# Optimization experiments

Hardware: AMD Instinct MI355X
Metric: run time of the kernel (lower is better)

The kernel has to match this reference:

```python
import jax, jax.numpy as jnp
import numpy as np

Q_BITS = 8
GELU_A = -0.2888
GELU_B = -1.769
INV_SQRT2 = 0.7071067811865476


def _ste_round(x):
    # straight-through round (identity grad)
    return x + jax.lax.stop_gradient(jnp.round(x) - x)


def fake_quant_weight(w):
    # per-tensor symmetric int8 fake quant
    qmax = 2.0 ** (Q_BITS - 1) - 1.0  # 127
    s = jnp.maximum(jnp.max(jnp.abs(w)), 1e-8) / qmax
    q = jnp.clip(_ste_round(w / s), -qmax - 1.0, qmax)
    return q * s


def fake_quant_act(x):
    # per-tensor asymmetric uint8 fake quant
    levels = 2.0 ** Q_BITS - 1.0  # 255
    xmin = jax.lax.stop_gradient(jnp.min(x))
    xmax = jax.lax.stop_gradient(jnp.max(x))
    s = jnp.maximum(xmax - xmin, 1e-8) / levels
    zp = jnp.round(-xmin / s)
    q = jnp.clip(_ste_round(x / s) + zp, 0.0, levels)
    return (q - zp) * s


def int_gelu(x):
    # I-BERT polynomial GELU: gelu(x) = x * 0.5 * (1 + L(x/sqrt(2)))
    # L(t) = sign(t) * (a * (clip(|t|, 0, -b) + b)^2 + 1)
    t = x * INV_SQRT2
    at = jnp.minimum(jnp.abs(t), -GELU_B)
    L = jnp.sign(t) * (GELU_A * (at + GELU_B) ** 2 + 1.0)
    return x * 0.5 * (1.0 + L)


def setup_inputs() -> dict:
    key = jax.random.key(0)
    k = jax.random.split(key, 5)
    B, S, D, H = 64, 197, 768, 3072
    x = jax.random.normal(k[0], (B, S, D), dtype=jnp.float32)
    w1 = jax.random.normal(k[1], (H, D), dtype=jnp.float32) * (1.0 / np.sqrt(D))
    b1 = jax.random.normal(k[2], (H,), dtype=jnp.float32) * 0.02
    w2 = jax.random.normal(k[3], (D, H), dtype=jnp.float32) * (1.0 / np.sqrt(H))
    b2 = jax.random.normal(k[4], (D,), dtype=jnp.float32) * 0.02
    return {"x": x, "w1": w1, "b1": b1, "w2": w2, "b2": b2}


def reference(x, w1, b1, w2, b2):
    # QuantLinear 1: fake-quant act + weight, then GEMM
    xq = fake_quant_act(x)
    h = jnp.einsum('bsd,hd->bsh', xq, fake_quant_weight(w1)) + b1
    # IntGELU (dropout is identity in eval)
    g = int_gelu(h)
    # QuantLinear 2
    gq = fake_quant_act(g)
    out = jnp.einsum('bsh,dh->bsd', gq, fake_quant_weight(w2)) + b2
    return out
```

## Files before the change

kernel.cpp:

```cpp
#include <hip/hip_runtime.h>
#include <stdint.h>
#include <stddef.h>

typedef int v4i  __attribute__((ext_vector_type(4)));
typedef int v16i __attribute__((ext_vector_type(16)));
typedef _Float16 vh8 __attribute__((ext_vector_type(8)));

#define GELU_A   (-0.2888f)
#define GELU_B   (-1.769f)
#define INV_SQRT2 0.70710678118654752440f

#define GLD16(gp, lp) __builtin_amdgcn_global_load_lds( \
    (const __attribute__((address_space(1))) unsigned int*)(gp), \
    (__attribute__((address_space(3))) unsigned int*)(lp), 16, 0, 0)

#define WAIT_VM4 0x0F74
#define WAIT_VM0 0x0F70


__device__ __forceinline__ unsigned enc_f(float f){
  unsigned u = __float_as_uint(f);
  return (u & 0x80000000u) ? ~u : (u | 0x80000000u);
}
__device__ __forceinline__ float dec_f(unsigned e){
  unsigned u = (e & 0x80000000u) ? (e & 0x7FFFFFFFu) : ~e;
  return __uint_as_float(u);
}

__device__ __forceinline__ float int_gelu_f(float x){
  float t = x * INV_SQRT2;
  float at = fminf(fabsf(t), 1.769f);
  float u = at + GELU_B;
  float p = GELU_A * (u * u) + 1.0f;
  float L = (t > 0.0f) ? p : ((t < 0.0f) ? -p : 0.0f);
  return x * 0.5f * (1.0f + L);
}

__global__ __launch_bounds__(256) void reduce_stats(
    const float4* __restrict__ x, int nx4,
    const float4* __restrict__ w1, int n14,
    const float4* __restrict__ w2, int n24,
    unsigned* __restrict__ sc)
{
  __shared__ float ra[256], rb[256];
  const int tid = threadIdx.x;
  const int b = blockIdx.x;
  if (b < 1024){
    float lmin = 3.4e38f, lmax = -3.4e38f;
    for (long i = (long)b * 256 + tid; i < nx4; i += 1024L * 256L){
      float4 v = x[i];
      lmin = fminf(lmin, fminf(fminf(v.x, v.y), fminf(v.z, v.w)));
      lmax = fmaxf(lmax, fmaxf(fmaxf(v.x, v.y), fmaxf(v.z, v.w)));
    }
    ra[tid] = lmin; rb[tid] = lmax;
    __syncthreads();
    for (int s = 128; s > 0; s >>= 1){
      if (tid < s){ ra[tid] = fminf(ra[tid], ra[tid + s]); rb[tid] = fmaxf(rb[tid], rb[tid + s]); }
      __syncthreads();
    }
    if (tid == 0){
      atomicMin(&sc[0], enc_f(ra[0]));
      atomicMax(&sc[2], enc_f(rb[0]));
    }
  } else {
    const float4* w; int n4; int slot; int bl;
    if (b < 1152){ w = w1; n4 = n14; slot = 3; bl = b - 1024; }
    else         { w = w2; n4 = n24; slot = 4; bl = b - 1152; }
    float la = 0.0f;
    for (long i = (long)bl * 256 + tid; i < n4; i += 128L * 256L){
      float4 v = w[i];
      la = fmaxf(la, fmaxf(fmaxf(fabsf(v.x), fabsf(v.y)), fmaxf(fabsf(v.z), fabsf(v.w))));
    }
    ra[tid] = la;
    __syncthreads();
    for (int s = 128; s > 0; s >>= 1){
      if (tid < s) ra[tid] = fmaxf(ra[tid], ra[tid + s]);
      __syncthreads();
    }
    if (tid == 0) atomicMax(&sc[slot], __float_as_uint(ra[0]));
  }
}

__global__ __launch_bounds__(256) void quant_all(
    const float4* __restrict__ x, unsigned* __restrict__ qx, long nx4,
    const float* __restrict__ w1, const float* __restrict__ w2,
    int8_t* __restrict__ qw1, int8_t* __restrict__ qw2,
    int* __restrict__ rs1, int* __restrict__ rs2,
    const unsigned* __restrict__ sc, int H, int D)
{
  const int tid = threadIdx.x;
  const int b = blockIdx.x;
  if (b < 2048){
    const float vmin = dec_f(sc[0]);
    const float vmax = dec_f(sc[2]);
    const float s  = fmaxf(vmax - vmin, 1e-8f) / 255.0f;
    const float zp = rintf(-vmin / s);
    for (long i = (long)b * 256 + tid; i < nx4; i += 2048L * 256L){
      float4 v = x[i];
      int q0 = (int)fminf(fmaxf(rintf(v.x / s) + zp, 0.0f), 255.0f) - 128;
      int q1 = (int)fminf(fmaxf(rintf(v.y / s) + zp, 0.0f), 255.0f) - 128;
      int q2 = (int)fminf(fmaxf(rintf(v.z / s) + zp, 0.0f), 255.0f) - 128;
      int q3 = (int)fminf(fmaxf(rintf(v.w / s) + zp, 0.0f), 255.0f) - 128;
      qx[i] = ((unsigned)(q0 & 255)) | ((unsigned)(q1 & 255) << 8) |
              ((unsigned)(q2 & 255) << 16) | ((unsigned)(q3 & 255) << 24);
    }
  } else {
    __shared__ int red[256];
    const int wb = b - 2048;
    const float* w; int8_t* q; int* rs; int K; int n; float s;
    if (wb < H){ w = w1; q = qw1; rs = rs1; K = D; n = wb;
                 s = fmaxf(__uint_as_float(sc[3]), 1e-8f) / 127.0f; }
    else       { w = w2; q = qw2; rs = rs2; K = H; n = wb - H;
                 s = fmaxf(__uint_as_float(sc[4]), 1e-8f) / 127.0f; }
    int sum = 0;
    for (int k = tid; k < K; k += 256){
      float v = w[(size_t)n * K + k];
      float qf = fminf(fmaxf(rintf(v / s), -128.0f), 127.0f);
      int qi = (int)qf;
      q[(size_t)n * K + k] = (int8_t)qi;
      sum += qi;
    }
    red[tid] = sum;
    __syncthreads();
    for (int st = 128; st > 0; st >>= 1){
      if (tid < st) red[tid] += red[tid + st];
      __syncthreads();
    }
    if (tid == 0) rs[n] = red[0];
  }
}

__global__ __launch_bounds__(256) void quant_g(
    const vh8* __restrict__ g, uint2* __restrict__ qg, long n8,
    const unsigned* __restrict__ sc)
{
  const float gmin = dec_f(sc[1]), gmax = dec_f(sc[5]);
  const float qs  = fmaxf(gmax - gmin, 1e-8f) / 255.0f;
  const float qzp = rintf(-gmin / qs);
  const long stride = (long)gridDim.x * blockDim.x;
  for (long i = (long)blockIdx.x * blockDim.x + threadIdx.x; i < n8; i += stride){
    vh8 v = g[i];
    unsigned lo = 0, hi = 0;
#pragma unroll
    for (int j = 0; j < 4; j++){
      int q = (int)fminf(fmaxf(rintf((float)v[j] / qs) + qzp, 0.0f), 255.0f) - 128;
      lo |= ((unsigned)(q & 255)) << (8 * j);
    }
#pragma unroll
    for (int j = 0; j < 4; j++){
      int q = (int)fminf(fmaxf(rintf((float)v[4 + j] / qs) + qzp, 0.0f), 255.0f) - 128;
      hi |= ((unsigned)(q & 255)) << (8 * j);
    }
    uint2 o; o.x = lo; o.y = hi;
    qg[i] = o;
  }
}

template<int MODE>
__global__ __launch_bounds__(256) void gemm_i8(
    const int8_t* __restrict__ A, const int8_t* __restrict__ Bm,
    const int* __restrict__ rowsum, const float* __restrict__ bias,
    void* __restrict__ Cout, int M, int N, int K,
    unsigned* __restrict__ sc)
{
  __shared__ __align__(16) int8_t lds[3][16384];

  const int tid  = threadIdx.x;
  const int lane = tid & 63;
  const int wave = tid >> 6;
  const int l31  = lane & 31;
  const int kh   = lane >> 5;
  const int n0   = blockIdx.x * 128;
  const int m0   = blockIdx.y * 128;
  const int wm   = (wave & 1) * 64;
  const int wn   = (wave >> 1) * 64;

  int aoffs[2], boffs[2];
  const int ldst[2] = { wave * 2048, wave * 2048 + 1024 };
#pragma unroll
  for (int t = 0; t < 2; t++){
    int rowl = wave * 32 + t * 16 + (lane >> 2);
    int csw  = ((lane & 3) ^ ((rowl >> 1) & 3)) << 4;
    int ga = m0 + rowl; if (ga >= M) ga = M - 1;
    aoffs[t] = ga * K + csw;
    boffs[t] = (n0 + rowl) * K + csw;
  }

  const int w2  = (l31 >> 1) & 3;
  const int sA0 = (kh ^ w2) << 4;
  int arow[2], brow[2];
#pragma unroll
  for (int mi = 0; mi < 2; mi++){
    arow[mi] = (wm + mi * 32 + l31) * 64;
    brow[mi] = (wn + mi * 32 + l31) * 64;
  }

  v16i acc[2][2] = {};
  const int NT = K >> 6;

#pragma unroll
  for (int t = 0; t < 2; t++){
    GLD16(A  + aoffs[t],      &lds[0][ldst[t]]);
    GLD16(Bm + boffs[t],      &lds[0][8192 + ldst[t]]);
  }
#pragma unroll
  for (int t = 0; t < 2; t++){
    GLD16(A  + aoffs[t] + 64, &lds[1][ldst[t]]);
    GLD16(Bm + boffs[t] + 64, &lds[1][8192 + ldst[t]]);
  }

  for (int kt = 0; kt < NT; kt++){
    const int8_t* buf = lds[kt % 3];
    if (kt + 1 < NT) __builtin_amdgcn_s_waitcnt(WAIT_VM4);
    else             __builtin_amdgcn_s_waitcnt(WAIT_VM0);
    __builtin_amdgcn_s_barrier();
    __builtin_amdgcn_sched_barrier(0);

    v4i af[2][2], bf[2][2];
#pragma unroll
    for (int kk = 0; kk < 2; kk++){
      const int sb = sA0 ^ (kk << 5);
#pragma unroll
      for (int mi = 0; mi < 2; mi++){
        af[kk][mi] = *(const v4i*)(buf + arow[mi] + sb);
        bf[kk][mi] = *(const v4i*)(buf + 8192 + brow[mi] + sb);
      }
    }

    if (kt + 2 < NT){
      int8_t* nbuf = lds[(kt + 2) % 3];
      const int ko = (kt + 2) << 6;
#pragma unroll
      for (int t = 0; t < 2; t++){
        GLD16(A  + aoffs[t] + ko, nbuf + ldst[t]);
        GLD16(Bm + boffs[t] + ko, nbuf + 8192 + ldst[t]);
      }
    }

#pragma unroll
    for (int kk = 0; kk < 2; kk++)
#pragma unroll
      for (int mi = 0; mi < 2; mi++)
#pragma unroll
        for (int nj = 0; nj < 2; nj++)
          acc[mi][nj] = __builtin_amdgcn_mfma_i32_32x32x32_i8(af[kk][mi], bf[kk][nj], acc[mi][nj], 0, 0, 0);
  }

  float s_h, off_h;
  if constexpr (MODE == 1){
    float gmin = dec_f(sc[1]), gmax = dec_f(sc[5]);
    float sg = fmaxf(gmax - gmin, 1e-8f) / 255.0f;
    float zp = rintf(-gmin / sg);
    float sw = fmaxf(__uint_as_float(sc[4]), 1e-8f) / 127.0f;
    s_h = sg * sw; off_h = 128.0f - zp;
  } else {
    float xmin = dec_f(sc[0]), xmax = dec_f(sc[2]);
    float sx = fmaxf(xmax - xmin, 1e-8f) / 255.0f;
    float zp = rintf(-xmin / sx);
    float sw = fmaxf(__uint_as_float(sc[3]), 1e-8f) / 127.0f;
    s_h = sx * sw; off_h = 128.0f - zp;
  }
  float qs = 1.0f, qzp = 0.0f;
  if constexpr (MODE == 2){
    float gmin = dec_f(sc[1]), gmax = dec_f(sc[5]);
    qs = fmaxf(gmax - gmin, 1e-8f) / 255.0f;
    qzp = rintf(-gmin / qs);
  }

  float lmin = 3.4e38f, lmax = -3.4e38f;
#pragma unroll
  for (int nj = 0; nj < 2; nj++){
    const int n = n0 + wn + nj * 32 + l31;
    const float rsv = off_h * (float)rowsum[n];
    const float bv = bias[n];
#pragma unroll
    for (int mi = 0; mi < 2; mi++){
      const int mbase = m0 + wm + mi * 32 + 4 * kh;
#pragma unroll
      for (int r = 0; r < 16; r++){
        const int m = mbase + (r & 3) + 8 * (r >> 2);
        if (m < M){
          float h = s_h * ((float)acc[mi][nj][r] + rsv) + bv;
          if constexpr (MODE == 0){
            float gv = int_gelu_f(h);
            lmin = fminf(lmin, gv); lmax = fmaxf(lmax, gv);
          } else if constexpr (MODE == 3){
            float gv = int_gelu_f(h);
            lmin = fminf(lmin, gv); lmax = fmaxf(lmax, gv);
            ((_Float16*)Cout)[(size_t)m * N + n] = (_Float16)gv;
          } else if constexpr (MODE == 2){
            float gv = int_gelu_f(h);
            float qf = fminf(fmaxf(rintf(gv / qs) + qzp, 0.0f), 255.0f);
            ((int8_t*)Cout)[(size_t)m * N + n] = (int8_t)((int)qf - 128);
          } else {
            ((float*)Cout)[(size_t)m * N + n] = h;
          }
        }
      }
    }
  }

  if constexpr (MODE == 0 || MODE == 3){
    __syncthreads();
    float* redA = (float*)&lds[0][0];
    float* redB = ((float*)&lds[0][0]) + 256;
    redA[tid] = lmin; redB[tid] = lmax;
    __syncthreads();
    for (int st = 128; st > 0; st >>= 1){
      if (tid < st){
        redA[tid] = fminf(redA[tid], redA[tid + st]);
        redB[tid] = fmaxf(redB[tid], redB[tid + st]);
      }
      __syncthreads();
    }
    if (tid == 0){
      atomicMin(&sc[1], enc_f(redA[0]));
      atomicMax(&sc[5], enc_f(redB[0]));
    }
  }
}

extern "C" void kernel_launch(void* const* d_in, const int* in_sizes, int n_in,
                              void* d_out, int out_size, void* d_ws, size_t ws_size,
                              hipStream_t stream)
{
  const float* x  = (const float*)d_in[0];
  const float* w1 = (const float*)d_in[1];
  const float* b1 = (const float*)d_in[2];
  const float* w2 = (const float*)d_in[3];
  const float* b2 = (const float*)d_in[4];
  float* out = (float*)d_out;

  const int H = in_sizes[2];
  const int D = in_sizes[4];
  const int M = in_sizes[0] / D;

  char* ws = (char*)d_ws;
  unsigned* sc = (unsigned*)ws;
  size_t off = 256;
  int8_t* qx  = (int8_t*)(ws + off); off += (size_t)M * D;
  int8_t* qw1 = (int8_t*)(ws + off); off += (size_t)H * D;
  int8_t* qw2 = (int8_t*)(ws + off); off += (size_t)D * H;
  int* rs1 = (int*)(ws + off); off += (size_t)H * 4;
  int* rs2 = (int*)(ws + off); off += 4096;
  int8_t* qg  = (int8_t*)(ws + off); off += (size_t)M * H;
  _Float16* g16 = (_Float16*)(ws + off);
  const size_t need_big = off + (size_t)M * H * 2;
  (void)n_in; (void)out_size;

  hipMemsetAsync(sc, 0xFF, 8, stream);
  hipMemsetAsync(sc + 2, 0x00, 16, stream);

  reduce_stats<<<dim3(1280), dim3(256), 0, stream>>>(
      (const float4*)x, M * D / 4,
      (const float4*)w1, H * D / 4,
      (const float4*)w2, D * H / 4, sc);

  quant_all<<<dim3(2048 + H + D), dim3(256), 0, stream>>>(
      (const float4*)x, (unsigned*)qx, (long)M * D / 4,
      w1, w2, qw1, qw2, rs1, rs2, sc, H, D);

  const dim3 g1(H / 128, (M + 127) / 128), g2(D / 128, (M + 127) / 128), blk(256);

  if (ws_size >= need_big){
    gemm_i8<3><<<g1, blk, 0, stream>>>(qx, qw1, rs1, b1, g16, M, H, D, sc);
    quant_g<<<dim3(2048), blk, 0, stream>>>(
        (const vh8*)g16, (uint2*)qg, (long)M * H / 8, sc);
  } else {
    gemm_i8<0><<<g1, blk, 0, stream>>>(qx, qw1, rs1, b1, nullptr, M, H, D, sc);
    gemm_i8<2><<<g1, blk, 0, stream>>>(qx, qw1, rs1, b1, qg, M, H, D, sc);
  }

  gemm_i8<1><<<g2, blk, 0, stream>>>(qg, qw2, rs2, b2, out, M, D, H, sc);
}
```

Before: 309.3 us.

## Widen int8 GEMM block tile to 128x256 with 64x128 per-wave subtiles

Doubles the N extent of each GEMM block tile from 128 to 256, so each wave computes a 64x128 output subtile with a 2x4 array of MFMA accumulators. B-tile loads per stage double and the LDS triple buffer grows to 24 KB per stage, with the vmcnt wait adjusted for the six outstanding loads. The aim is more reuse of each A fragment and a higher MFMA-to-LDS-read ratio. In exchange the grid is half as large, accumulator register use doubles, and occupancy may drop, which could leave CUs idle on the 768-wide second GEMM.

```diff
diff --git a/kernel.cpp b/kernel.cpp
--- a/kernel.cpp
+++ b/kernel.cpp
@@ -14,7 +14,7 @@
     (const __attribute__((address_space(1))) unsigned int*)(gp), \
     (__attribute__((address_space(3))) unsigned int*)(lp), 16, 0, 0)
 
-#define WAIT_VM4 0x0F74
+#define WAIT_VM6 0x0F76
 #define WAIT_VM0 0x0F70
 
 
@@ -157,84 +157,88 @@
 }
 
 template<int MODE>
-__global__ __launch_bounds__(256) void gemm_i8(
+__global__ __launch_bounds__(256, 2) void gemm_i8(
     const int8_t* __restrict__ A, const int8_t* __restrict__ Bm,
     const int* __restrict__ rowsum, const float* __restrict__ bias,
     void* __restrict__ Cout, int M, int N, int K,
     unsigned* __restrict__ sc)
 {
-  __shared__ __align__(16) int8_t lds[3][16384];
+  __shared__ __align__(16) int8_t lds[3][24576];
 
   const int tid  = threadIdx.x;
   const int lane = tid & 63;
   const int wave = tid >> 6;
   const int l31  = lane & 31;
   const int kh   = lane >> 5;
-  const int n0   = blockIdx.x * 128;
+  const int n0   = blockIdx.x * 256;
   const int m0   = blockIdx.y * 128;
-  const int wm   = (wave & 1) * 64;
-  const int wn   = (wave >> 1) * 64;
-
-  int aoffs[2], boffs[2];
-  const int ldst[2] = { wave * 2048, wave * 2048 + 1024 };
+  const int wm   = (wave >> 1) * 64;
+  const int wn   = (wave & 1) * 128;
+
+  int aoffs[2], boffs[4];
+  const int ldstA[2] = { wave * 2048, wave * 2048 + 1024 };
+  const int ldstB[4] = { 8192 + wave * 4096,        8192 + wave * 4096 + 1024,
+                         8192 + wave * 4096 + 2048, 8192 + wave * 4096 + 3072 };
 #pragma unroll
   for (int t = 0; t < 2; t++){
     int rowl = wave * 32 + t * 16 + (lane >> 2);
     int csw  = ((lane & 3) ^ ((rowl >> 1) & 3)) << 4;
     int ga = m0 + rowl; if (ga >= M) ga = M - 1;
     aoffs[t] = ga * K + csw;
+  }
+#pragma unroll
+  for (int t = 0; t < 4; t++){
+    int rowl = wave * 64 + t * 16 + (lane >> 2);
+    int csw  = ((lane & 3) ^ ((rowl >> 1) & 3)) << 4;
     boffs[t] = (n0 + rowl) * K + csw;
   }
 
   const int w2  = (l31 >> 1) & 3;
   const int sA0 = (kh ^ w2) << 4;
-  int arow[2], brow[2];
-#pragma unroll
-  for (int mi = 0; mi < 2; mi++){
-    arow[mi] = (wm + mi * 32 + l31) * 64;
-    brow[mi] = (wn + mi * 32 + l31) * 64;
-  }
-
-  v16i acc[2][2] = {};
+  int arow[2], brow[4];
+#pragma unroll
+  for (int mi = 0; mi < 2; mi++) arow[mi] = (wm + mi * 32 + l31) * 64;
+#pragma unroll
+  for (int nj = 0; nj < 4; nj++) brow[nj] = (wn + nj * 32 + l31) * 64;
+
+  v16i acc[2][4] = {};
   const int NT = K >> 6;
 
 #pragma unroll
-  for (int t = 0; t < 2; t++){
-    GLD16(A  + aoffs[t],      &lds[0][ldst[t]]);
-    GLD16(Bm + boffs[t],      &lds[0][8192 + ldst[t]]);
-  }
-#pragma unroll
-  for (int t = 0; t < 2; t++){
-    GLD16(A  + aoffs[t] + 64, &lds[1][ldst[t]]);
-    GLD16(Bm + boffs[t] + 64, &lds[1][8192 + ldst[t]]);
-  }
+  for (int t = 0; t < 2; t++) GLD16(A  + aoffs[t],      &lds[0][ldstA[t]]);
+#pragma unroll
+  for (int t = 0; t < 4; t++) GLD16(Bm + boffs[t],      &lds[0][ldstB[t]]);
+#pragma unroll
+  for (int t = 0; t < 2; t++) GLD16(A  + aoffs[t] + 64, &lds[1][ldstA[t]]);
+#pragma unroll
+  for (int t = 0; t < 4; t++) GLD16(Bm + boffs[t] + 64, &lds[1][ldstB[t]]);
 
   for (int kt = 0; kt < NT; kt++){
     const int8_t* buf = lds[kt % 3];
-    if (kt + 1 < NT) __builtin_amdgcn_s_waitcnt(WAIT_VM4);
+    if (kt + 1 < NT) __builtin_amdgcn_s_waitcnt(WAIT_VM6);
     else             __builtin_amdgcn_s_waitcnt(WAIT_VM0);
     __builtin_amdgcn_s_barrier();
     __builtin_amdgcn_sched_barrier(0);
 
-    v4i af[2][2], bf[2][2];
+    v4i af[2][2], bf[2][4];
 #pragma unroll
     for (int kk = 0; kk < 2; kk++){
       const int sb = sA0 ^ (kk << 5);
 #pragma unroll
-      for (int mi = 0; mi < 2; mi++){
+      for (int mi = 0; mi < 2; mi++)
         af[kk][mi] = *(const v4i*)(buf + arow[mi] + sb);
-        bf[kk][mi] = *(const v4i*)(buf + 8192 + brow[mi] + sb);
-      }
+#pragma unroll
+      for (int nj = 0; nj < 4; nj++)
+        bf[kk][nj] = *(const v4i*)(buf + 8192 + brow[nj] + sb);
     }
 
     if (kt + 2 < NT){
       int8_t* nbuf = lds[(kt + 2) % 3];
       const int ko = (kt + 2) << 6;
 #pragma unroll
-      for (int t = 0; t < 2; t++){
-        GLD16(A  + aoffs[t] + ko, nbuf + ldst[t]);
-        GLD16(Bm + boffs[t] + ko, nbuf + 8192 + ldst[t]);
-      }
+      for (int t = 0; t < 2; t++) GLD16(A  + aoffs[t] + ko, nbuf + ldstA[t]);
+#pragma unroll
+      for (int t = 0; t < 4; t++) GLD16(Bm + boffs[t] + ko, nbuf + ldstB[t]);
     }
 
 #pragma unroll
@@ -242,7 +246,7 @@
 #pragma unroll
       for (int mi = 0; mi < 2; mi++)
 #pragma unroll
-        for (int nj = 0; nj < 2; nj++)
+        for (int nj = 0; nj < 4; nj++)
           acc[mi][nj] = __builtin_amdgcn_mfma_i32_32x32x32_i8(af[kk][mi], bf[kk][nj], acc[mi][nj], 0, 0, 0);
   }
 
@@ -269,7 +273,7 @@
 
   float lmin = 3.4e38f, lmax = -3.4e38f;
 #pragma unroll
-  for (int nj = 0; nj < 2; nj++){
+  for (int nj = 0; nj < 4; nj++){
     const int n = n0 + wn + nj * 32 + l31;
     const float rsv = off_h * (float)rowsum[n];
     const float bv = bias[n];
@@ -360,7 +364,7 @@
       (const float4*)x, (unsigned*)qx, (long)M * D / 4,
       w1, w2, qw1, qw2, rs1, rs2, sc, H, D);
 
-  const dim3 g1(H / 128, (M + 127) / 128), g2(D / 128, (M + 127) / 128), blk(256);
+  const dim3 g1(H / 256, (M + 127) / 128), g2(D / 256, (M + 127) / 128), blk(256);
 
   if (ws_size >= need_big){
     gemm_i8<3><<<g1, blk, 0, stream>>>(qx, qw1, rs1, b1, g16, M, H, D, sc);
```

New measurement: 331.8 us. 7.3% more time.

## Pre-swizzle int8 operands into MFMA fragment layout and drop LDS staging

Applied to the files above, without the earlier changes.

Quantization kernels now write activations, weights and the intermediate GELU output in a blocked 32x32 fragment-native layout. This lets the GEMM load each lane's MFMA operands directly from global memory with 16-byte loads, removing the LDS triple-buffer, global-to-LDS copies and barriers. The K loop is double-buffered in registers and occupancy is hinted with launch bounds. The trade-off is that each wave reads its operands directly from global memory with no LDS sharing, so reuse depends on caches, and there is less latency hiding than with the LDS pipeline.

```diff
diff --git a/kernel.cpp b/kernel.cpp
--- a/kernel.cpp
+++ b/kernel.cpp
@@ -10,12 +10,6 @@
 #define GELU_B   (-1.769f)
 #define INV_SQRT2 0.70710678118654752440f
 
-#define GLD16(gp, lp) __builtin_amdgcn_global_load_lds( \
-    (const __attribute__((address_space(1))) unsigned int*)(gp), \
-    (__attribute__((address_space(3))) unsigned int*)(lp), 16, 0, 0)
-
-#define WAIT_VM4 0x0F74
-#define WAIT_VM0 0x0F70
 
 
 __device__ __forceinline__ unsigned enc_f(float f){
@@ -81,8 +75,17 @@
   }
 }
 
+__device__ __forceinline__ unsigned quant4_act(float4 v, float s, float zp){
+  int q0 = (int)fminf(fmaxf(rintf(v.x / s) + zp, 0.0f), 255.0f) - 128;
+  int q1 = (int)fminf(fmaxf(rintf(v.y / s) + zp, 0.0f), 255.0f) - 128;
+  int q2 = (int)fminf(fmaxf(rintf(v.z / s) + zp, 0.0f), 255.0f) - 128;
+  int q3 = (int)fminf(fmaxf(rintf(v.w / s) + zp, 0.0f), 255.0f) - 128;
+  return ((unsigned)(q0 & 255)) | ((unsigned)(q1 & 255) << 8) |
+         ((unsigned)(q2 & 255) << 16) | ((unsigned)(q3 & 255) << 24);
+}
+
 __global__ __launch_bounds__(256) void quant_all(
-    const float4* __restrict__ x, unsigned* __restrict__ qx, long nx4,
+    const float* __restrict__ x, int8_t* __restrict__ qx, long nchunk,
     const float* __restrict__ w1, const float* __restrict__ w2,
     int8_t* __restrict__ qw1, int8_t* __restrict__ qw2,
     int* __restrict__ rs1, int* __restrict__ rs2,
@@ -95,14 +98,19 @@
     const float vmax = dec_f(sc[2]);
     const float s  = fmaxf(vmax - vmin, 1e-8f) / 255.0f;
     const float zp = rintf(-vmin / s);
-    for (long i = (long)b * 256 + tid; i < nx4; i += 2048L * 256L){
-      float4 v = x[i];
-      int q0 = (int)fminf(fmaxf(rintf(v.x / s) + zp, 0.0f), 255.0f) - 128;
-      int q1 = (int)fminf(fmaxf(rintf(v.y / s) + zp, 0.0f), 255.0f) - 128;
-      int q2 = (int)fminf(fmaxf(rintf(v.z / s) + zp, 0.0f), 255.0f) - 128;
-      int q3 = (int)fminf(fmaxf(rintf(v.w / s) + zp, 0.0f), 255.0f) - 128;
-      qx[i] = ((unsigned)(q0 & 255)) | ((unsigned)(q1 & 255) << 8) |
-              ((unsigned)(q2 & 255) << 16) | ((unsigned)(q3 & 255) << 24);
+    const long CPR = (long)(D >> 4);
+    const long KB  = (long)(D >> 5);
+    for (long i = (long)b * 256 + tid; i < nchunk; i += 2048L * 256L){
+      long m = i / CPR; int c = (int)(i - m * CPR);
+      const float4* xp = (const float4*)(x + m * (long)D + (long)c * 16);
+      uint4 o;
+      o.x = quant4_act(xp[0], s, zp);
+      o.y = quant4_act(xp[1], s, zp);
+      o.z = quant4_act(xp[2], s, zp);
+      o.w = quant4_act(xp[3], s, zp);
+      size_t off = ((((size_t)(m >> 5)) * KB + (c >> 1)) << 10)
+                 + ((size_t)(c & 1) << 9) + ((m & 31) << 4);
+      *(uint4*)(qx + off) = o;
     }
   } else {
     __shared__ int red[256];
@@ -113,12 +121,25 @@
     else       { w = w2; q = qw2; rs = rs2; K = H; n = wb - H;
                  s = fmaxf(__uint_as_float(sc[4]), 1e-8f) / 127.0f; }
     int sum = 0;
-    for (int k = tid; k < K; k += 256){
-      float v = w[(size_t)n * K + k];
-      float qf = fminf(fmaxf(rintf(v / s), -128.0f), 127.0f);
-      int qi = (int)qf;
-      q[(size_t)n * K + k] = (int8_t)qi;
-      sum += qi;
+    const int c = tid;
+    if (c < (K >> 4)){
+      const float4* wp = (const float4*)(w + (size_t)n * K + (size_t)c * 16);
+      uint4 o; unsigned wds[4];
+#pragma unroll
+      for (int q4 = 0; q4 < 4; q4++){
+        float4 v = wp[q4];
+        int qa = (int)fminf(fmaxf(rintf(v.x / s), -128.0f), 127.0f);
+        int qb = (int)fminf(fmaxf(rintf(v.y / s), -128.0f), 127.0f);
+        int qc = (int)fminf(fmaxf(rintf(v.z / s), -128.0f), 127.0f);
+        int qd = (int)fminf(fmaxf(rintf(v.w / s), -128.0f), 127.0f);
+        sum += qa + qb + qc + qd;
+        wds[q4] = ((unsigned)(qa & 255)) | ((unsigned)(qb & 255) << 8) |
+                  ((unsigned)(qc & 255) << 16) | ((unsigned)(qd & 255) << 24);
+      }
+      o.x = wds[0]; o.y = wds[1]; o.z = wds[2]; o.w = wds[3];
+      size_t off = ((((size_t)(n >> 5)) * (K >> 5) + (c >> 1)) << 10)
+                 + ((size_t)(c & 1) << 9) + ((n & 31) << 4);
+      *(uint4*)(q + off) = o;
     }
     red[tid] = sum;
     __syncthreads();
@@ -131,40 +152,38 @@
 }
 
 __global__ __launch_bounds__(256) void quant_g(
-    const vh8* __restrict__ g, uint2* __restrict__ qg, long n8,
+    const vh8* __restrict__ gf, uint4* __restrict__ qg, long nchunk,
     const unsigned* __restrict__ sc)
 {
   const float gmin = dec_f(sc[1]), gmax = dec_f(sc[5]);
   const float qs  = fmaxf(gmax - gmin, 1e-8f) / 255.0f;
   const float qzp = rintf(-gmin / qs);
   const long stride = (long)gridDim.x * blockDim.x;
-  for (long i = (long)blockIdx.x * blockDim.x + threadIdx.x; i < n8; i += stride){
-    vh8 v = g[i];
-    unsigned lo = 0, hi = 0;
-#pragma unroll
-    for (int j = 0; j < 4; j++){
-      int q = (int)fminf(fmaxf(rintf((float)v[j] / qs) + qzp, 0.0f), 255.0f) - 128;
-      lo |= ((unsigned)(q & 255)) << (8 * j);
-    }
-#pragma unroll
-    for (int j = 0; j < 4; j++){
-      int q = (int)fminf(fmaxf(rintf((float)v[4 + j] / qs) + qzp, 0.0f), 255.0f) - 128;
-      hi |= ((unsigned)(q & 255)) << (8 * j);
-    }
-    uint2 o; o.x = lo; o.y = hi;
+  for (long i = (long)blockIdx.x * blockDim.x + threadIdx.x; i < nchunk; i += stride){
+    vh8 v0 = gf[2 * i], v1 = gf[2 * i + 1];
+    unsigned wds[4] = {0u, 0u, 0u, 0u};
+#pragma unroll
+    for (int j = 0; j < 8; j++){
+      int q = (int)fminf(fmaxf(rintf((float)v0[j] / qs) + qzp, 0.0f), 255.0f) - 128;
+      wds[j >> 2] |= ((unsigned)(q & 255)) << (8 * (j & 3));
+    }
+#pragma unroll
+    for (int j = 0; j < 8; j++){
+      int q = (int)fminf(fmaxf(rintf((float)v1[j] / qs) + qzp, 0.0f), 255.0f) - 128;
+      wds[2 + (j >> 2)] |= ((unsigned)(q & 255)) << (8 * (j & 3));
+    }
+    uint4 o; o.x = wds[0]; o.y = wds[1]; o.z = wds[2]; o.w = wds[3];
     qg[i] = o;
   }
 }
 
 template<int MODE>
-__global__ __launch_bounds__(256) void gemm_i8(
-    const int8_t* __restrict__ A, const int8_t* __restrict__ Bm,
+__global__ __launch_bounds__(256, 4) void gemm_i8f(
+    const int8_t* __restrict__ Af, const int8_t* __restrict__ Bf,
     const int* __restrict__ rowsum, const float* __restrict__ bias,
     void* __restrict__ Cout, int M, int N, int K,
     unsigned* __restrict__ sc)
 {
-  __shared__ __align__(16) int8_t lds[3][16384];
-
   const int tid  = threadIdx.x;
   const int lane = tid & 63;
   const int wave = tid >> 6;
@@ -174,76 +193,51 @@
   const int m0   = blockIdx.y * 128;
   const int wm   = (wave & 1) * 64;
   const int wn   = (wave >> 1) * 64;
-
-  int aoffs[2], boffs[2];
-  const int ldst[2] = { wave * 2048, wave * 2048 + 1024 };
-#pragma unroll
-  for (int t = 0; t < 2; t++){
-    int rowl = wave * 32 + t * 16 + (lane >> 2);
-    int csw  = ((lane & 3) ^ ((rowl >> 1) & 3)) << 4;
-    int ga = m0 + rowl; if (ga >= M) ga = M - 1;
-    aoffs[t] = ga * K + csw;
-    boffs[t] = (n0 + rowl) * K + csw;
-  }
-
-  const int w2  = (l31 >> 1) & 3;
-  const int sA0 = (kh ^ w2) << 4;
-  int arow[2], brow[2];
+  const int NKB  = K >> 5;
+  const int MBmax = (M >> 5) - 1;
+
+  const int8_t* apt[2]; const int8_t* bpt[2];
 #pragma unroll
   for (int mi = 0; mi < 2; mi++){
-    arow[mi] = (wm + mi * 32 + l31) * 64;
-    brow[mi] = (wn + mi * 32 + l31) * 64;
+    int rb = (m0 + wm + mi * 32) >> 5; if (rb > MBmax) rb = MBmax;
+    apt[mi] = Af + ((size_t)rb * NKB) * 1024 + lane * 16;
+  }
+#pragma unroll
+  for (int nj = 0; nj < 2; nj++){
+    int cb = (n0 + wn + nj * 32) >> 5;
+    bpt[nj] = Bf + ((size_t)cb * NKB) * 1024 + lane * 16;
   }
 
   v16i acc[2][2] = {};
-  const int NT = K >> 6;
-
-#pragma unroll
-  for (int t = 0; t < 2; t++){
-    GLD16(A  + aoffs[t],      &lds[0][ldst[t]]);
-    GLD16(Bm + boffs[t],      &lds[0][8192 + ldst[t]]);
-  }
-#pragma unroll
-  for (int t = 0; t < 2; t++){
-    GLD16(A  + aoffs[t] + 64, &lds[1][ldst[t]]);
-    GLD16(Bm + boffs[t] + 64, &lds[1][8192 + ldst[t]]);
-  }
-
-  for (int kt = 0; kt < NT; kt++){
-    const int8_t* buf = lds[kt % 3];
-    if (kt + 1 < NT) __builtin_amdgcn_s_waitcnt(WAIT_VM4);
-    else             __builtin_amdgcn_s_waitcnt(WAIT_VM0);
-    __builtin_amdgcn_s_barrier();
-    __builtin_amdgcn_sched_barrier(0);
-
-    v4i af[2][2], bf[2][2];
-#pragma unroll
-    for (int kk = 0; kk < 2; kk++){
-      const int sb = sA0 ^ (kk << 5);
-#pragma unroll
-      for (int mi = 0; mi < 2; mi++){
-        af[kk][mi] = *(const v4i*)(buf + arow[mi] + sb);
-        bf[kk][mi] = *(const v4i*)(buf + 8192 + brow[mi] + sb);
-      }
-    }
-
-    if (kt + 2 < NT){
-      int8_t* nbuf = lds[(kt + 2) % 3];
-      const int ko = (kt + 2) << 6;
-#pragma unroll
-      for (int t = 0; t < 2; t++){
-        GLD16(A  + aoffs[t] + ko, nbuf + ldst[t]);
-        GLD16(Bm + boffs[t] + ko, nbuf + 8192 + ldst[t]);
-      }
-    }
-
-#pragma unroll
-    for (int kk = 0; kk < 2; kk++)
-#pragma unroll
-      for (int mi = 0; mi < 2; mi++)
-#pragma unroll
-        for (int nj = 0; nj < 2; nj++)
-          acc[mi][nj] = __builtin_amdgcn_mfma_i32_32x32x32_i8(af[kk][mi], bf[kk][nj], acc[mi][nj], 0, 0, 0);
+  v4i a0[2], b0[2], a1[2], b1[2];
+#pragma unroll
+  for (int mi = 0; mi < 2; mi++) a0[mi] = *(const v4i*)(apt[mi]);
+#pragma unroll
+  for (int nj = 0; nj < 2; nj++) b0[nj] = *(const v4i*)(bpt[nj]);
+
+  for (int kb = 0; kb < NKB; kb += 2){
+    const size_t o1 = (size_t)(kb + 1) << 10;
+    const size_t o2 = (size_t)(kb + 2) << 10;
+#pragma unroll
+    for (int mi = 0; mi < 2; mi++) a1[mi] = *(const v4i*)(apt[mi] + o1);
+#pragma unroll
+    for (int nj = 0; nj < 2; nj++) b1[nj] = *(const v4i*)(bpt[nj] + o1);
+#pragma unroll
+    for (int mi = 0; mi < 2; mi++)
+#pragma unroll
+      for (int nj = 0; nj < 2; nj++)
+        acc[mi][nj] = __builtin_amdgcn_mfma_i32_32x32x32_i8(a0[mi], b0[nj], acc[mi][nj], 0, 0, 0);
+    if (kb + 2 < NKB){
+#pragma unroll
+      for (int mi = 0; mi < 2; mi++) a0[mi] = *(const v4i*)(apt[mi] + o2);
+#pragma unroll
+      for (int nj = 0; nj < 2; nj++) b0[nj] = *(const v4i*)(bpt[nj] + o2);
+    }
+#pragma unroll
+    for (int mi = 0; mi < 2; mi++)
+#pragma unroll
+      for (int nj = 0; nj < 2; nj++)
+        acc[mi][nj] = __builtin_amdgcn_mfma_i32_32x32x32_i8(a1[mi], b1[nj], acc[mi][nj], 0, 0, 0);
   }
 
   float s_h, off_h;
@@ -287,11 +281,15 @@
           } else if constexpr (MODE == 3){
             float gv = int_gelu_f(h);
             lmin = fminf(lmin, gv); lmax = fmaxf(lmax, gv);
-            ((_Float16*)Cout)[(size_t)m * N + n] = (_Float16)gv;
+            size_t hidx = ((((size_t)(m >> 5)) * (N >> 5) + (n >> 5)) << 10)
+                        + ((size_t)((n >> 4) & 1) << 9) + ((m & 31) << 4) + (n & 15);
+            ((_Float16*)Cout)[hidx] = (_Float16)gv;
           } else if constexpr (MODE == 2){
             float gv = int_gelu_f(h);
             float qf = fminf(fmaxf(rintf(gv / qs) + qzp, 0.0f), 255.0f);
-            ((int8_t*)Cout)[(size_t)m * N + n] = (int8_t)((int)qf - 128);
+            size_t bidx = ((((size_t)(m >> 5)) * (N >> 5) + (n >> 5)) << 10)
+                        + ((size_t)((n >> 4) & 1) << 9) + ((m & 31) << 4) + (n & 15);
+            ((int8_t*)Cout)[bidx] = (int8_t)((int)qf - 128);
           } else {
             ((float*)Cout)[(size_t)m * N + n] = h;
           }
@@ -301,9 +299,7 @@
   }
 
   if constexpr (MODE == 0 || MODE == 3){
-    __syncthreads();
-    float* redA = (float*)&lds[0][0];
-    float* redB = ((float*)&lds[0][0]) + 256;
+    __shared__ float redA[256], redB[256];
     redA[tid] = lmin; redB[tid] = lmax;
     __syncthreads();
     for (int st = 128; st > 0; st >>= 1){
@@ -357,19 +353,19 @@
       (const float4*)w2, D * H / 4, sc);
 
   quant_all<<<dim3(2048 + H + D), dim3(256), 0, stream>>>(
-      (const float4*)x, (unsigned*)qx, (long)M * D / 4,
+      x, qx, (long)M * D / 16,
       w1, w2, qw1, qw2, rs1, rs2, sc, H, D);
 
   const dim3 g1(H / 128, (M + 127) / 128), g2(D / 128, (M + 127) / 128), blk(256);
 
   if (ws_size >= need_big){
-    gemm_i8<3><<<g1, blk, 0, stream>>>(qx, qw1, rs1, b1, g16, M, H, D, sc);
-    quant_g<<<dim3(2048), blk, 0, stream>>>(
-        (const vh8*)g16, (uint2*)qg, (long)M * H / 8, sc);
+    gemm_i8f<3><<<g1, blk, 0, stream>>>(qx, qw1, rs1, b1, g16, M, H, D, sc);
+    quant_g<<<dim3(2048), dim3(256), 0, stream>>>(
+        (const vh8*)g16, (uint4*)qg, (long)M * H / 16, sc);
   } else {
-    gemm_i8<0><<<g1, blk, 0, stream>>>(qx, qw1, rs1, b1, nullptr, M, H, D, sc);
-    gemm_i8<2><<<g1, blk, 0, stream>>>(qx, qw1, rs1, b1, qg, M, H, D, sc);
-  }
-
-  gemm_i8<1><<<g2, blk, 0, stream>>>(qg, qw2, rs2, b2, out, M, D, H, sc);
-}
+    gemm_i8f<0><<<g1, blk, 0, stream>>>(qx, qw1, rs1, b1, nullptr, M, H, D, sc);
+    gemm_i8f<2><<<g1, blk, 0, stream>>>(qx, qw1, rs1, b1, qg, M, H, D, sc);
+  }
+
+  gemm_i8f<1><<<g2, blk, 0, stream>>>(qg, qw2, rs2, b2, out, M, D, H, sc);
+}
```

Result: slower. 327.7 us (+6.0%).

## Enlarge int8 GEMM tiles to 256x256 with 8 waves and double-buffered K=128 stages

Applied to the files above, without the earlier changes.

Replaces the 128x128 tile, 4-wave, triple-buffered K=64 int8 MFMA GEMM with a 256x256 tile, 512-thread kernel. Each wave computes a 128x64 sub-tile. The kernel double-buffers 128-wide K slices in 128KB of LDS, swizzles over 8 16-byte chunks, and adds explicit barriers plus s_setprio around the MFMA clusters. The goal is more data reuse per global byte and a higher ratio of MFMA work to loads. The costs are fewer blocks, with the N=768 GEMM getting only 3 column tiles, more barriers per K step, and a large LDS footprint that limits occupancy.

```diff
diff --git a/kernel.cpp b/kernel.cpp
--- a/kernel.cpp
+++ b/kernel.cpp
@@ -14,8 +14,8 @@
     (const __attribute__((address_space(1))) unsigned int*)(gp), \
     (__attribute__((address_space(3))) unsigned int*)(lp), 16, 0, 0)
 
-#define WAIT_VM4 0x0F74
-#define WAIT_VM0 0x0F70
+#define WAIT_VM0   0x0F70
+#define WAIT_LGKM0 0xC07F
 
 
 __device__ __forceinline__ unsigned enc_f(float f){
@@ -157,93 +157,100 @@
 }
 
 template<int MODE>
-__global__ __launch_bounds__(256) void gemm_i8(
+__global__ __launch_bounds__(512, 2) void gemm_i8p(
     const int8_t* __restrict__ A, const int8_t* __restrict__ Bm,
     const int* __restrict__ rowsum, const float* __restrict__ bias,
     void* __restrict__ Cout, int M, int N, int K,
     unsigned* __restrict__ sc)
 {
-  __shared__ __align__(16) int8_t lds[3][16384];
+  __shared__ __align__(16) int8_t lds[2][65536];
 
   const int tid  = threadIdx.x;
   const int lane = tid & 63;
   const int wave = tid >> 6;
   const int l31  = lane & 31;
   const int kh   = lane >> 5;
-  const int n0   = blockIdx.x * 128;
-  const int m0   = blockIdx.y * 128;
-  const int wm   = (wave & 1) * 64;
-  const int wn   = (wave >> 1) * 64;
-
-  int aoffs[2], boffs[2];
-  const int ldst[2] = { wave * 2048, wave * 2048 + 1024 };
-#pragma unroll
-  for (int t = 0; t < 2; t++){
-    int rowl = wave * 32 + t * 16 + (lane >> 2);
-    int csw  = ((lane & 3) ^ ((rowl >> 1) & 3)) << 4;
-    int ga = m0 + rowl; if (ga >= M) ga = M - 1;
-    aoffs[t] = ga * K + csw;
-    boffs[t] = (n0 + rowl) * K + csw;
-  }
-
-  const int w2  = (l31 >> 1) & 3;
-  const int sA0 = (kh ^ w2) << 4;
-  int arow[2], brow[2];
-#pragma unroll
-  for (int mi = 0; mi < 2; mi++){
-    arow[mi] = (wm + mi * 32 + l31) * 64;
-    brow[mi] = (wn + mi * 32 + l31) * 64;
-  }
-
-  v16i acc[2][2] = {};
-  const int NT = K >> 6;
-
-#pragma unroll
-  for (int t = 0; t < 2; t++){
-    GLD16(A  + aoffs[t],      &lds[0][ldst[t]]);
-    GLD16(Bm + boffs[t],      &lds[0][8192 + ldst[t]]);
-  }
-#pragma unroll
-  for (int t = 0; t < 2; t++){
-    GLD16(A  + aoffs[t] + 64, &lds[1][ldst[t]]);
-    GLD16(Bm + boffs[t] + 64, &lds[1][8192 + ldst[t]]);
-  }
-
-  for (int kt = 0; kt < NT; kt++){
-    const int8_t* buf = lds[kt % 3];
-    if (kt + 1 < NT) __builtin_amdgcn_s_waitcnt(WAIT_VM4);
-    else             __builtin_amdgcn_s_waitcnt(WAIT_VM0);
-    __builtin_amdgcn_s_barrier();
-    __builtin_amdgcn_sched_barrier(0);
-
-    v4i af[2][2], bf[2][2];
-#pragma unroll
-    for (int kk = 0; kk < 2; kk++){
-      const int sb = sA0 ^ (kk << 5);
-#pragma unroll
-      for (int mi = 0; mi < 2; mi++){
-        af[kk][mi] = *(const v4i*)(buf + arow[mi] + sb);
-        bf[kk][mi] = *(const v4i*)(buf + 8192 + brow[mi] + sb);
+  const int n0   = blockIdx.x * 256;
+  const int m0   = blockIdx.y * 256;
+  const int wm   = (wave >> 2) * 128;
+  const int wn   = (wave & 3) * 64;
+  const int NT   = K >> 7;
+
+  int aoff[4], boff[4], ldsoA[4], ldsoB[4];
+#pragma unroll
+  for (int i = 0; i < 4; i++){
+    const int h = i >> 1, q = i & 1;
+    const int r0 = wave * 16 + q * 8;
+    const int r  = r0 + (lane >> 3);
+    const int cs = (lane & 7) ^ ((r >> 1) & 7);
+    int ga = m0 + h * 128 + r; if (ga >= M) ga = M - 1;
+    aoff[i] = ga * K + cs * 16;
+    boff[i] = (n0 + h * 128 + r) * K + cs * 16;
+    ldsoA[i] = h * 16384 + r0 * 128;
+    ldsoB[i] = 32768 + h * 16384 + r0 * 128;
+  }
+
+  int raddrA[4], rswzA[4], raddrB[2], rswzB[2];
+#pragma unroll
+  for (int mi = 0; mi < 4; mi++){
+    const int row = wm + mi * 32 + l31;
+    raddrA[mi] = (row >> 7) * 16384 + (row & 127) * 128;
+    rswzA[mi]  = ((row & 127) >> 1) & 7;
+  }
+#pragma unroll
+  for (int nj = 0; nj < 2; nj++){
+    const int row = wn + nj * 32 + l31;
+    raddrB[nj] = 32768 + (row >> 7) * 16384 + (row & 127) * 128;
+    rswzB[nj]  = ((row & 127) >> 1) & 7;
+  }
+
+  v16i acc[4][2] = {};
+
+#pragma unroll
+  for (int i = 0; i < 4; i++) GLD16(A  + aoff[i], &lds[0][ldsoA[i]]);
+#pragma unroll
+  for (int i = 0; i < 4; i++) GLD16(Bm + boff[i], &lds[0][ldsoB[i]]);
+  __builtin_amdgcn_s_waitcnt(WAIT_VM0);
+  __builtin_amdgcn_s_barrier();
+
+  for (int t = 0; t < NT; t++){
+    const int8_t* buf = &lds[t & 1][0];
+    int8_t* nbuf = &lds[(t + 1) & 1][0];
+    const bool pf = (t + 1 < NT);
+    const int ko = (t + 1) << 7;
+
+#pragma unroll
+    for (int kb = 0; kb < 4; kb++){
+      v4i af[4], bf[2];
+      const int ch = kb * 2 + kh;
+#pragma unroll
+      for (int mi = 0; mi < 4; mi++)
+        af[mi] = *(const v4i*)(buf + raddrA[mi] + ((ch ^ rswzA[mi]) << 4));
+#pragma unroll
+      for (int nj = 0; nj < 2; nj++)
+        bf[nj] = *(const v4i*)(buf + raddrB[nj] + ((ch ^ rswzB[nj]) << 4));
+
+      if (kb == 0 && pf){
+#pragma unroll
+        for (int i = 0; i < 4; i++) GLD16(A  + aoff[i] + ko, nbuf + ldsoA[i]);
+#pragma unroll
+        for (int i = 0; i < 4; i++) GLD16(Bm + boff[i] + ko, nbuf + ldsoB[i]);
       }
-    }
-
-    if (kt + 2 < NT){
-      int8_t* nbuf = lds[(kt + 2) % 3];
-      const int ko = (kt + 2) << 6;
-#pragma unroll
-      for (int t = 0; t < 2; t++){
-        GLD16(A  + aoffs[t] + ko, nbuf + ldst[t]);
-        GLD16(Bm + boffs[t] + ko, nbuf + 8192 + ldst[t]);
-      }
-    }
-
-#pragma unroll
-    for (int kk = 0; kk < 2; kk++)
-#pragma unroll
-      for (int mi = 0; mi < 2; mi++)
+      __builtin_amdgcn_sched_barrier(0);
+      if (kb == 3) __builtin_amdgcn_s_waitcnt(WAIT_VM0);
+      __builtin_amdgcn_s_barrier();
+      __builtin_amdgcn_s_waitcnt(WAIT_LGKM0);
+      __builtin_amdgcn_sched_barrier(0);
+      __builtin_amdgcn_s_setprio(1);
+#pragma unroll
+      for (int mi = 0; mi < 4; mi++)
 #pragma unroll
         for (int nj = 0; nj < 2; nj++)
-          acc[mi][nj] = __builtin_amdgcn_mfma_i32_32x32x32_i8(af[kk][mi], bf[kk][nj], acc[mi][nj], 0, 0, 0);
+          acc[mi][nj] = __builtin_amdgcn_mfma_i32_32x32x32_i8(af[mi], bf[nj], acc[mi][nj], 0, 0, 0);
+      __builtin_amdgcn_s_setprio(0);
+      __builtin_amdgcn_sched_barrier(0);
+      __builtin_amdgcn_s_barrier();
+    }
   }
 
   float s_h, off_h;
@@ -274,7 +281,7 @@
     const float rsv = off_h * (float)rowsum[n];
     const float bv = bias[n];
 #pragma unroll
-    for (int mi = 0; mi < 2; mi++){
+    for (int mi = 0; mi < 4; mi++){
       const int mbase = m0 + wm + mi * 32 + 4 * kh;
 #pragma unroll
       for (int r = 0; r < 16; r++){
@@ -303,10 +310,10 @@
   if constexpr (MODE == 0 || MODE == 3){
     __syncthreads();
     float* redA = (float*)&lds[0][0];
-    float* redB = ((float*)&lds[0][0]) + 256;
+    float* redB = ((float*)&lds[0][0]) + 512;
     redA[tid] = lmin; redB[tid] = lmax;
     __syncthreads();
-    for (int st = 128; st > 0; st >>= 1){
+    for (int st = 256; st > 0; st >>= 1){
       if (tid < st){
         redA[tid] = fminf(redA[tid], redA[tid + st]);
         redB[tid] = fmaxf(redB[tid], redB[tid + st]);
@@ -360,16 +367,16 @@
       (const float4*)x, (unsigned*)qx, (long)M * D / 4,
       w1, w2, qw1, qw2, rs1, rs2, sc, H, D);
 
-  const dim3 g1(H / 128, (M + 127) / 128), g2(D / 128, (M + 127) / 128), blk(256);
+  const dim3 g1(H / 256, (M + 255) / 256), g2(D / 256, (M + 255) / 256), blk(512);
 
   if (ws_size >= need_big){
-    gemm_i8<3><<<g1, blk, 0, stream>>>(qx, qw1, rs1, b1, g16, M, H, D, sc);
-    quant_g<<<dim3(2048), blk, 0, stream>>>(
+    gemm_i8p<3><<<g1, blk, 0, stream>>>(qx, qw1, rs1, b1, g16, M, H, D, sc);
+    quant_g<<<dim3(2048), dim3(256), 0, stream>>>(
         (const vh8*)g16, (uint2*)qg, (long)M * H / 8, sc);
   } else {
-    gemm_i8<0><<<g1, blk, 0, stream>>>(qx, qw1, rs1, b1, nullptr, M, H, D, sc);
-    gemm_i8<2><<<g1, blk, 0, stream>>>(qx, qw1, rs1, b1, qg, M, H, D, sc);
-  }
-
-  gemm_i8<1><<<g2, blk, 0, stream>>>(qg, qw2, rs2, b2, out, M, D, H, sc);
-}
+    gemm_i8p<0><<<g1, blk, 0, stream>>>(qx, qw1, rs1, b1, nullptr, M, H, D, sc);
+    gemm_i8p<2><<<g1, blk, 0, stream>>>(qx, qw1, rs1, b1, qg, M, H, D, sc);
+  }
+
+  gemm_i8p<1><<<g2, blk, 0, stream>>>(qg, qw2, rs2, b2, out, M, D, H, sc);
+}
```

New measurement: 337.1 us. 1.09x slower.
